# Kernel optimization log

Hardware: AMD Instinct MI355X
Metric: run time of the kernel (lower is better)

## Reference

```python
import jax, jax.numpy as jnp
import numpy as np

N = 100_000        # num nodes
E = 1_600_000      # num edges (self-loops appended in reference)
IN_DIM = 128
OUT_DIM = 128
NUM_HEAD = 8
D_HEAD = OUT_DIM // NUM_HEAD
NEG_SLOPE = 0.2
EPS = 1e-10


def setup_inputs() -> dict:
    key = jax.random.key(0)
    k1, k2, k3, k4, k5 = jax.random.split(key, 5)
    x = jax.random.normal(k1, (N, IN_DIM), dtype=jnp.float32)
    edge_list = jax.random.randint(k2, (E, 2), 0, N, dtype=jnp.int32)
    edge_weight = jax.random.uniform(k3, (E,), dtype=jnp.float32)
    # nn.Linear(input_dim, output_dim) params
    W = jax.random.normal(k4, (IN_DIM, OUT_DIM), dtype=jnp.float32) / np.sqrt(IN_DIM).astype(np.float32)
    b = jnp.zeros((OUT_DIM,), dtype=jnp.float32)
    # query: (num_head, 2*output_dim/num_head), kaiming-uniform-ish init
    query = jax.random.normal(k5, (NUM_HEAD, 2 * D_HEAD), dtype=jnp.float32) * 0.1
    return {"x": x, "edge_list": edge_list, "edge_weight": edge_weight,
            "W": W, "b": b, "query": query}


def reference(x, edge_list, edge_weight, W, b, query):
    # --- message ---
    self_idx = jnp.arange(N, dtype=edge_list.dtype)
    node_in = jnp.concatenate([edge_list[:, 0], self_idx])   # [E+N]
    node_out = jnp.concatenate([edge_list[:, 1], self_idx])  # [E+N]
    ew = jnp.concatenate([edge_weight, jnp.ones((N,), edge_weight.dtype)])[:, None]  # [E+N,1]

    hidden = x @ W + b                                        # [N, OUT_DIM]
    h_in = hidden[node_in]                                    # [E+N, OUT_DIM]
    h_out = hidden[node_out]                                  # [E+N, OUT_DIM]

    # torch: stack(..., dim=-1).view(-1, num_head, 2*d_head) -> interleaved layout
    key_ = jnp.stack([h_in, h_out], axis=-1).reshape(-1, NUM_HEAD, 2 * D_HEAD)
    w = jnp.einsum('hd,nhd->nh', query, key_)                 # [E+N, H]
    w = jax.nn.leaky_relu(w, NEG_SLOPE)

    seg_max = jax.ops.segment_max(w, node_out, num_segments=N)  # [N, H]
    w = w - seg_max[node_out]
    att = jnp.exp(w) * ew                                     # [E+N, H]

    counts = jax.ops.segment_sum(jnp.ones((node_out.shape[0],), att.dtype),
                                 node_out, num_segments=N)[:, None]  # [N,1] (>=1: self-loops)
    norm = jax.ops.segment_sum(att, node_out, num_segments=N) / counts  # scatter_mean
    att = att / (norm[node_out] + EPS)

    value = h_in.reshape(-1, NUM_HEAD, D_HEAD)
    message = (att[..., None] * value).reshape(-1, OUT_DIM)   # [E+N, OUT_DIM]

    # --- aggregate: scatter_mean over node_out ---
    update = jax.ops.segment_sum(message, node_out, num_segments=N) / counts

    # --- combine: relu activation, no batch norm ---
    return jax.nn.relu(update)
```

## Files before the change

kernel.cpp:

```cpp
#include <hip/hip_runtime.h>

#define NH 8
#define DH 16
#define OD 128
#define NCH 256
#define NPB 128
#define ECAP 3072

typedef __attribute__((ext_vector_type(8))) short bf16x8;
typedef __attribute__((ext_vector_type(4))) float f32x4;

__device__ inline unsigned int f2bf(float f) {
    unsigned int u = __float_as_uint(f);
    return (u + 0x7fffu + ((u >> 16) & 1u)) >> 16;
}


__global__ __launch_bounds__(256) void binhist_kernel(const int2* __restrict__ el,
                                                      int* __restrict__ cnt,
                                                      int E, int total, int CH, int NB) {
    __shared__ int lh[1024];
    int t = threadIdx.x, c = blockIdx.x;
    for (int i = t; i < NB; i += 256) lh[i] = 0;
    __syncthreads();
    int beg = c * CH, end = min(total, beg + CH);
    for (int i = beg + t; i < end; i += 256) {
        int dst = (i < E) ? el[i].y : (i - E);
        atomicAdd(&lh[dst >> 7], 1);
    }
    __syncthreads();
    for (int i = t; i < NB; i += 256) cnt[i * NCH + c] = lh[i];
}

__global__ __launch_bounds__(1024) void scan1_kernel(const int* __restrict__ counts,
                                                     int* __restrict__ offsets,
                                                     int* __restrict__ bsums, int n) {
    __shared__ int tmp[1024];
    int t = threadIdx.x;
    int gid = blockIdx.x * 1024 + t;
    int v = (gid < n) ? counts[gid] : 0;
    tmp[t] = v;
    __syncthreads();
    int val = v;
    for (int off = 1; off < 1024; off <<= 1) {
        int add = (t >= off) ? tmp[t - off] : 0;
        __syncthreads();
        val += add;
        tmp[t] = val;
        __syncthreads();
    }
    if (gid < n) offsets[gid] = val - v;
    if (t == 1023) bsums[blockIdx.x] = val;
}

__global__ __launch_bounds__(1024) void scan2_kernel(int* __restrict__ bsums, int nb) {
    __shared__ int tmp[1024];
    int t = threadIdx.x;
    int v = (t < nb) ? bsums[t] : 0;
    tmp[t] = v;
    __syncthreads();
    int val = v;
    for (int off = 1; off < 1024; off <<= 1) {
        int add = (t >= off) ? tmp[t - off] : 0;
        __syncthreads();
        val += add;
        tmp[t] = val;
        __syncthreads();
    }
    if (t < nb) bsums[t] = val - v;
}

__global__ __launch_bounds__(1024) void scan3b_kernel(int* __restrict__ S,
                                                      const int* __restrict__ bsums,
                                                      const int* __restrict__ cnt, int n) {
    int gid = blockIdx.x * 1024 + threadIdx.x;
    if (gid < n) {
        int o = S[gid] + bsums[gid >> 10];
        S[gid] = o;
        if (gid == n - 1) S[n] = o + cnt[gid];
    }
}

__global__ __launch_bounds__(256) void binscatter_kernel(const int2* __restrict__ el,
                                                         const float* __restrict__ ew,
                                                         const int* __restrict__ S,
                                                         int2* __restrict__ binned,
                                                         int E, int total, int CH, int NB) {
    __shared__ int lcur[1024];
    int t = threadIdx.x, c = blockIdx.x;
    for (int i = t; i < NB; i += 256) lcur[i] = S[i * NCH + c];
    __syncthreads();
    int beg = c * CH, end = min(total, beg + CH);
    for (int i = beg + t; i < end; i += 256) {
        int src, dst; float w;
        if (i < E) { int2 e = el[i]; src = e.x; dst = e.y; w = ew[i]; }
        else       { src = dst = i - E; w = 1.0f; }
        int b = dst >> 7;
        int pos = atomicAdd(&lcur[b], 1);
        binned[pos] = make_int2(src | ((dst & 127) << 17), __float_as_int(w));
    }
}

__global__ __launch_bounds__(256) void binsort_kernel(const int2* __restrict__ binned,
                                                      const int* __restrict__ S,
                                                      int2* __restrict__ sedge,
                                                      int* __restrict__ offsets,
                                                      int N, int NB, int total) {
    __shared__ int2 eb[ECAP];
    __shared__ int lh[NPB];
    __shared__ int cu[NPB];
    int b = blockIdx.x, t = threadIdx.x;
    int base = S[b * NCH];
    int endb = S[(b + 1) * NCH];
    int cnt = min(endb - base, ECAP);

    for (int i = t; i < NPB; i += 256) lh[i] = 0;
    __syncthreads();
    for (int i = t; i < cnt; i += 256) {
        int2 e = binned[base + i];
        eb[i] = e;
        atomicAdd(&lh[(e.x >> 17) & 127], 1);
    }
    __syncthreads();
    if (t < 64) {
        int loc[2]; int s = 0;
#pragma unroll
        for (int j = 0; j < 2; ++j) { loc[j] = lh[t * 2 + j]; s += loc[j]; }
        int inc = s;
        for (int d = 1; d < 64; d <<= 1) {
            int o = __shfl_up(inc, d, 64);
            if (t >= d) inc += o;
        }
        int ex = inc - s;
#pragma unroll
        for (int j = 0; j < 2; ++j) { cu[t * 2 + j] = ex; ex += loc[j]; }
    }
    __syncthreads();
    int node0 = b << 7;
    for (int i = t; i < NPB; i += 256) {
        int node = node0 + i;
        if (node < N) offsets[node] = base + cu[i];
    }
    if (b == NB - 1 && t == 0) offsets[N] = total;
    __syncthreads();
    for (int i = t; i < cnt; i += 256) {
        int2 e = eb[i];
        int d = (e.x >> 17) & 127;
        int pos = atomicAdd(&cu[d], 1);
        sedge[base + pos] = make_int2(e.x & 0x1FFFF, e.y);
    }
}

__global__ __launch_bounds__(256) void gemm_proj_kernel(
        const float* __restrict__ x, const float* __restrict__ W,
        const float* __restrict__ b, const float* __restrict__ query,
        unsigned short* __restrict__ hbu, float* __restrict__ ain,
        float* __restrict__ aout, int N) {
    __shared__ unsigned short xs[64 * 136];
    __shared__ unsigned short wt[128 * 136];
    int t = threadIdx.x;
    int row0 = blockIdx.x * 64;

    {
        const float4* x4 = (const float4*)x;
#pragma unroll
        for (int i = 0; i < 8; ++i) {
            int f = t + i * 256;
            int row = f >> 5, c4 = f & 31;
            int gr = row0 + row;
            if (gr >= N) gr = N - 1;
            float4 v = x4[(size_t)gr * 32 + c4];
            unsigned int u0 = f2bf(v.x) | (f2bf(v.y) << 16);
            unsigned int u1 = f2bf(v.z) | (f2bf(v.w) << 16);
            *(uint2*)&xs[row * 136 + 4 * c4] = make_uint2(u0, u1);
        }
    }
    {
        const float4* W4 = (const float4*)W;
#pragma unroll
        for (int i = 0; i < 16; ++i) {
            int f = t + i * 256;
            int k = f & 127, c4 = f >> 7;
            float4 v = W4[k * 32 + c4];
            wt[(4 * c4 + 0) * 136 + k] = (unsigned short)f2bf(v.x);
            wt[(4 * c4 + 1) * 136 + k] = (unsigned short)f2bf(v.y);
            wt[(4 * c4 + 2) * 136 + k] = (unsigned short)f2bf(v.z);
            wt[(4 * c4 + 3) * 136 + k] = (unsigned short)f2bf(v.w);
        }
    }
    __syncthreads();

    int lane = t & 63, wv = t >> 6;
    int d = lane & 15, g = lane >> 4;
    int tbase = wv * 16;

    bf16x8 af[4];
#pragma unroll
    for (int s = 0; s < 4; ++s)
        af[s] = *(bf16x8*)&xs[(tbase + d) * 136 + s * 32 + g * 8];

    f32x4 acc[8];
#pragma unroll
    for (int c = 0; c < 8; ++c) acc[c] = (f32x4){0.f, 0.f, 0.f, 0.f};

#pragma unroll
    for (int c = 0; c < 8; ++c) {
#pragma unroll
        for (int s = 0; s < 4; ++s) {
            bf16x8 bf = *(bf16x8*)&wt[(d + 16 * c) * 136 + s * 32 + g * 8];
            acc[c] = __builtin_amdgcn_mfma_f32_16x16x32_bf16(af[s], bf, acc[c], 0, 0, 0);
        }
    }

    int rbase = row0 + tbase + g * 4;
#pragma unroll
    for (int c = 0; c < 8; ++c) {
        float bc = b[d + 16 * c];
        float2 q2 = *(const float2*)(query + c * 2 * DH + 2 * d);
#pragma unroll
        for (int j = 0; j < 4; ++j) {
            float v = acc[c][j] + bc;
            int row = rbase + j;
            if (row < N) hbu[(size_t)row * OD + d + 16 * c] = (unsigned short)f2bf(v);
            float pin = q2.x * v, pout = q2.y * v;
#pragma unroll
            for (int m = 1; m < 16; m <<= 1) {
                pin  += __shfl_xor(pin, m, 64);
                pout += __shfl_xor(pout, m, 64);
            }
            if (d == 0 && row < N) {
                ain[row * NH + c] = pin;
                aout[row * NH + c] = pout;
            }
        }
    }
}

__global__ __launch_bounds__(256) void aggregate_kernel(
        const int* __restrict__ offsets, const int2* __restrict__ sedge,
        const float* __restrict__ ain, const float* __restrict__ aout,
        const unsigned int* __restrict__ hb, float* __restrict__ out, int N) {
    int n = (blockIdx.x * blockDim.x + threadIdx.x) >> 6;
    int lane = threadIdx.x & 63;
    if (n >= N) return;
    int beg = offsets[n], end = offsets[n + 1];
    int h = lane >> 3, s = lane & 7;
    int gbase = lane & 56;
    float ao = aout[n * NH + h];

    float ssum = 0.0f;
    float2 acc = make_float2(0.0f, 0.0f);
    for (int i = beg; i < end; i += 8) {
        int idx = i + s;
        float att = 0.0f;
        int src = 0;
        if (idx < end) {
            int2 e = sedge[idx];
            src = e.x;
            float a = ain[src * NH + h] + ao;
            a = (a > 0.0f) ? a : 0.2f * a;
            att = __expf(a) * __int_as_float(e.y);
        }
        ssum += att;
#pragma unroll
        for (int ss = 0; ss < 8; ++ss) {
            if (i + ss >= end) break;
            float att_s = __shfl(att, gbase | ss, 64);
            int src_s = __shfl(src, gbase | ss, 64);
            unsigned int vv = hb[(size_t)src_s * 64 + lane];
            acc.x += att_s * __uint_as_float(vv << 16);
            acc.y += att_s * __uint_as_float(vv & 0xffff0000u);
        }
    }
    ssum += __shfl_xor(ssum, 1, 64);
    ssum += __shfl_xor(ssum, 2, 64);
    ssum += __shfl_xor(ssum, 4, 64);

    float c = (float)(end - beg);
    float scale = 1.0f / ((ssum / c + 1e-10f) * c);
    float o0 = acc.x * scale, o1 = acc.y * scale;
    *(float2*)(out + (size_t)n * OD + 2 * lane) =
        make_float2(o0 > 0.0f ? o0 : 0.0f, o1 > 0.0f ? o1 : 0.0f);
}

extern "C" void kernel_launch(void* const* d_in, const int* in_sizes, int n_in,
                              void* d_out, int out_size, void* d_ws, size_t ws_size,
                              hipStream_t stream) {
    const float* x     = (const float*)d_in[0];
    const int2*  el    = (const int2*)d_in[1];
    const float* ew    = (const float*)d_in[2];
    const float* W     = (const float*)d_in[3];
    const float* b     = (const float*)d_in[4];
    const float* query = (const float*)d_in[5];
    float* out = (float*)d_out;

    int N = in_sizes[0] / OD;
    int E = in_sizes[1] / 2;
    int total = E + N;
    int NB = (N + NPB - 1) / NPB;
    int CH = (total + NCH - 1) / NCH;
    int n2 = NB * NCH;

    char* ws = (char*)d_ws;
    size_t off = 0;
    auto take = [&](size_t bytes) -> void* {
        void* p = ws + off;
        off = (off + bytes + 255) & ~(size_t)255;
        return p;
    };
    unsigned int* hb = (unsigned int*)take((size_t)N * 64 * 4);
    float* ain     = (float*)take((size_t)N * NH * 4);
    float* aout    = (float*)take((size_t)N * NH * 4);
    int*   cnt     = (int*)take((size_t)n2 * 4);
    int*   S       = (int*)take((size_t)(n2 + 1) * 4);
    int*   offsets = (int*)take((size_t)(N + 1) * 4);
    int*   bsums   = (int*)take(4096);
    int2*  binned  = (int2*)take((size_t)total * 8);
    int2*  sedge   = (int2*)take((size_t)total * 8);

    binhist_kernel<<<NCH, 256, 0, stream>>>(el, cnt, E, total, CH, NB);
    int nb = (n2 + 1023) / 1024;
    scan1_kernel<<<nb, 1024, 0, stream>>>(cnt, S, bsums, n2);
    scan2_kernel<<<1, 1024, 0, stream>>>(bsums, nb);
    scan3b_kernel<<<nb, 1024, 0, stream>>>(S, bsums, cnt, n2);
    binscatter_kernel<<<NCH, 256, 0, stream>>>(el, ew, S, binned, E, total, CH, NB);
    binsort_kernel<<<NB, 256, 0, stream>>>(binned, S, sedge, offsets, N, NB, total);
    gemm_proj_kernel<<<(N + 63) / 64, 256, 0, stream>>>(
        x, W, b, query, (unsigned short*)hb, ain, aout, N);
    aggregate_kernel<<<((size_t)N * 64 + 255) / 256, 256, 0, stream>>>(
        offsets, sedge, ain, aout, hb, out, N);
}
```

Baseline: 233.1 us.

## Split attention computation into per-bin edge kernel and simplify gather aggregation

A new edgeatt kernel computes per-edge attention weights once, stores them as bf16 in a head-major array, accumulates per-node softmax normalizers in shared memory, and writes a compact source-index array and per-node scale. The aggregate kernel then only gathers hidden rows with 8-byte loads, processing two edges per half-wave and combining the halves with a shuffle, which removes per-edge exp and shuffle work from the gather loop. This costs an extra kernel launch plus extra global traffic for the attention and source arrays. Storing attention in bf16 adds rounding error, and the aggregate loop reads srcArr past the segment end when the edge count is not a multiple of four.

Result: slower. 317.7 us (+36.3%).

```diff
diff --git a/kernel.cpp b/kernel.cpp
--- a/kernel.cpp
+++ b/kernel.cpp
@@ -147,7 +147,7 @@
         int2 e = eb[i];
         int d = (e.x >> 17) & 127;
         int pos = atomicAdd(&cu[d], 1);
-        sedge[base + pos] = make_int2(e.x & 0x1FFFF, e.y);
+        sedge[base + pos] = e;
     }
 }
 
@@ -236,51 +236,93 @@
     }
 }
 
+__global__ __launch_bounds__(256) void edgeatt_kernel(
+        const int* __restrict__ S, const int2* __restrict__ sedge,
+        const int* __restrict__ offsets, const float* __restrict__ ain,
+        const float* __restrict__ aout, unsigned short* __restrict__ attB,
+        int* __restrict__ srcArr, float* __restrict__ scaleG,
+        int N, int totalE) {
+    __shared__ float aoutL[NPB * NH];
+    __shared__ float normL[NPB * NH];
+    int b = blockIdx.x, t = threadIdx.x;
+    int base = S[b * NCH], end = S[(b + 1) * NCH];
+    int node0 = b * NPB;
+
+    for (int i = t; i < NPB * NH; i += 256) normL[i] = 0.0f;
+    ((float4*)aoutL)[t] = ((const float4*)aout)[(size_t)node0 * 2 + t];
+    __syncthreads();
+
+    int h = t >> 5, ii = t & 31;
+    size_t hbase = (size_t)h * totalE;
+    for (int i0 = base; i0 < end; i0 += 32) {
+        int idx = i0 + ii;
+        if (idx < end) {
+            int2 e = sedge[idx];
+            int src = e.x & 0x1FFFF, dl = (e.x >> 17) & 127;
+            float a = ain[src * NH + h] + aoutL[dl * NH + h];
+            a = (a > 0.0f) ? a : 0.2f * a;
+            float att = __expf(a) * __int_as_float(e.y);
+            attB[hbase + idx] = (unsigned short)f2bf(att);
+            atomicAdd(&normL[dl * NH + h], att);
+            if (h == 0) srcArr[idx] = src;
+        }
+    }
+    __syncthreads();
+    for (int j = t; j < NPB * NH; j += 256) {
+        int node = node0 + (j >> 3);
+        if (node < N) {
+            float c = (float)(offsets[node + 1] - offsets[node]);
+            float sm = normL[j];
+            scaleG[node * NH + (j & 7)] = 1.0f / ((sm / c + 1e-10f) * c);
+        }
+    }
+}
+
 __global__ __launch_bounds__(256) void aggregate_kernel(
-        const int* __restrict__ offsets, const int2* __restrict__ sedge,
-        const float* __restrict__ ain, const float* __restrict__ aout,
-        const unsigned int* __restrict__ hb, float* __restrict__ out, int N) {
+        const int* __restrict__ offsets, const int* __restrict__ srcArr,
+        const unsigned short* __restrict__ attB, const float* __restrict__ scaleG,
+        const uint2* __restrict__ hb2, float* __restrict__ out,
+        int N, int totalE) {
     int n = (blockIdx.x * blockDim.x + threadIdx.x) >> 6;
     int lane = threadIdx.x & 63;
     if (n >= N) return;
     int beg = offsets[n], end = offsets[n + 1];
-    int h = lane >> 3, s = lane & 7;
-    int gbase = lane & 56;
-    float ao = aout[n * NH + h];
-
-    float ssum = 0.0f;
-    float2 acc = make_float2(0.0f, 0.0f);
-    for (int i = beg; i < end; i += 8) {
-        int idx = i + s;
-        float att = 0.0f;
-        int src = 0;
-        if (idx < end) {
-            int2 e = sedge[idx];
-            src = e.x;
-            float a = ain[src * NH + h] + ao;
-            a = (a > 0.0f) ? a : 0.2f * a;
-            att = __expf(a) * __int_as_float(e.y);
-        }
-        ssum += att;
-#pragma unroll
-        for (int ss = 0; ss < 8; ++ss) {
-            if (i + ss >= end) break;
-            float att_s = __shfl(att, gbase | ss, 64);
-            int src_s = __shfl(src, gbase | ss, 64);
-            unsigned int vv = hb[(size_t)src_s * 64 + lane];
-            acc.x += att_s * __uint_as_float(vv << 16);
-            acc.y += att_s * __uint_as_float(vv & 0xffff0000u);
-        }
-    }
-    ssum += __shfl_xor(ssum, 1, 64);
-    ssum += __shfl_xor(ssum, 2, 64);
-    ssum += __shfl_xor(ssum, 4, 64);
-
-    float c = (float)(end - beg);
-    float scale = 1.0f / ((ssum / c + 1e-10f) * c);
-    float o0 = acc.x * scale, o1 = acc.y * scale;
-    *(float2*)(out + (size_t)n * OD + 2 * lane) =
-        make_float2(o0 > 0.0f ? o0 : 0.0f, o1 > 0.0f ? o1 : 0.0f);
+    int half = lane >> 5, q = lane & 31;
+    int h = q >> 2;
+    const unsigned short* attRow = attB + (size_t)h * totalE;
+
+    float4 acc = make_float4(0.f, 0.f, 0.f, 0.f);
+    for (int i = beg; i < end; i += 4) {
+        int ib = i + 2 * half;
+        int s0 = srcArr[ib] & 0x1FFFF;
+        int s1 = srcArr[ib + 1] & 0x1FFFF;
+        float a0 = (ib < end)     ? __uint_as_float((unsigned int)attRow[ib] << 16)     : 0.0f;
+        float a1 = (ib + 1 < end) ? __uint_as_float((unsigned int)attRow[ib + 1] << 16) : 0.0f;
+        uint2 w0 = hb2[(size_t)s0 * 32 + q];
+        uint2 w1 = hb2[(size_t)s1 * 32 + q];
+        acc.x += a0 * __uint_as_float(w0.x << 16);
+        acc.y += a0 * __uint_as_float(w0.x & 0xffff0000u);
+        acc.z += a0 * __uint_as_float(w0.y << 16);
+        acc.w += a0 * __uint_as_float(w0.y & 0xffff0000u);
+        acc.x += a1 * __uint_as_float(w1.x << 16);
+        acc.y += a1 * __uint_as_float(w1.x & 0xffff0000u);
+        acc.z += a1 * __uint_as_float(w1.y << 16);
+        acc.w += a1 * __uint_as_float(w1.y & 0xffff0000u);
+    }
+    acc.x += __shfl_xor(acc.x, 32, 64);
+    acc.y += __shfl_xor(acc.y, 32, 64);
+    acc.z += __shfl_xor(acc.z, 32, 64);
+    acc.w += __shfl_xor(acc.w, 32, 64);
+    if (half == 0) {
+        float sc = scaleG[n * NH + h];
+        float4 o;
+        o.x = acc.x * sc; o.y = acc.y * sc; o.z = acc.z * sc; o.w = acc.w * sc;
+        o.x = o.x > 0.f ? o.x : 0.f;
+        o.y = o.y > 0.f ? o.y : 0.f;
+        o.z = o.z > 0.f ? o.z : 0.f;
+        o.w = o.w > 0.f ? o.w : 0.f;
+        *(float4*)(out + (size_t)n * OD + 4 * q) = o;
+    }
 }
 
 extern "C" void kernel_launch(void* const* d_in, const int* in_sizes, int n_in,
@@ -310,13 +352,16 @@
     };
     unsigned int* hb = (unsigned int*)take((size_t)N * 64 * 4);
     float* ain     = (float*)take((size_t)N * NH * 4);
-    float* aout    = (float*)take((size_t)N * NH * 4);
+    float* aout    = (float*)take((size_t)(N + NPB) * NH * 4);
     int*   cnt     = (int*)take((size_t)n2 * 4);
     int*   S       = (int*)take((size_t)(n2 + 1) * 4);
     int*   offsets = (int*)take((size_t)(N + 1) * 4);
     int*   bsums   = (int*)take(4096);
     int2*  binned  = (int2*)take((size_t)total * 8);
     int2*  sedge   = (int2*)take((size_t)total * 8);
+    unsigned short* attB = (unsigned short*)take(((size_t)total * NH + 16) * 2);
+    int*   srcArr  = (int*)binned;
+    float* scaleG  = (float*)((char*)binned + ((size_t)total + 16) * 4);
 
     binhist_kernel<<<NCH, 256, 0, stream>>>(el, cnt, E, total, CH, NB);
     int nb = (n2 + 1023) / 1024;
@@ -327,6 +372,8 @@
     binsort_kernel<<<NB, 256, 0, stream>>>(binned, S, sedge, offsets, N, NB, total);
     gemm_proj_kernel<<<(N + 63) / 64, 256, 0, stream>>>(
         x, W, b, query, (unsigned short*)hb, ain, aout, N);
+    edgeatt_kernel<<<NB, 256, 0, stream>>>(
+        S, sedge, offsets, ain, aout, attB, srcArr, scaleG, N, total);
     aggregate_kernel<<<((size_t)N * 64 + 255) / 256, 256, 0, stream>>>(
-        offsets, sedge, ain, aout, hb, out, N);
-}
+        offsets, srcArr, attB, scaleG, (const uint2*)hb, out, N, total);
+}
```
